# Kernel tuning notes

Measured on AMD Instinct MI355X. Metric: run time of the kernel, lower is better.

The kernel has to match this reference:

```python
import jax, jax.numpy as jnp
import numpy as np
import math

DIM = 1024
CHUNK = 64
B, S = 4, 4096

def setup_inputs() -> dict:
    key = jax.random.key(0)
    ks = jax.random.split(key, 16)
    d = DIM
    std = 1.0 / math.sqrt(d)
    def lin(k):
        k1, k2 = jax.random.split(k)
        return (jax.random.uniform(k1, (d, d), jnp.float32, -std, std),
                jax.random.uniform(k2, (d,), jnp.float32, -std, std))
    Wk, bk = lin(ks[0])
    Wv, bv = lin(ks[1])
    Wq, bq = lin(ks[2])
    Wkp, bkp = lin(ks[3])
    Wqp, bqp = lin(ks[4])
    Wo, bo = lin(ks[5])
    return {
        "x": jax.random.normal(ks[6], (B, S, d), jnp.float32),
        "Wk": Wk, "bk": bk, "Wv": Wv, "bv": bv, "Wq": Wq, "bq": bq,
        "Wkp": Wkp, "bkp": bkp, "Wqp": Wqp, "bqp": bqp,
        "phase_scale": jnp.full((d,), math.pi, jnp.float32),
        "ln_g": jnp.ones((d,), jnp.float32),
        "ln_b": jnp.zeros((d,), jnp.float32),
        "Wo": Wo, "bo": bo,
    }

def _linear(x, W, b):
    # torch nn.Linear: x @ W.T + b
    return jnp.einsum('bsd,ed->bse', x, W) + b

def _layernorm(x, g, b, eps=1e-5):
    mu = jnp.mean(x, axis=-1, keepdims=True)
    var = jnp.var(x, axis=-1, keepdims=True)
    return (x - mu) * jax.lax.rsqrt(var + eps) * g + b

def reference(x, Wk, bk, Wv, bv, Wq, bq, Wkp, bkp, Wqp, bqp,
              phase_scale, ln_g, ln_b, Wo, bo):
    batch, seq_len, dim = x.shape
    key = _linear(x, Wk, bk)
    value = _linear(x, Wv, bv)
    query = _linear(x, Wq, bq)
    key_phase = jnp.tanh(_linear(key, Wkp, bkp)) * phase_scale
    query_phase = jnp.tanh(_linear(query, Wqp, bqp)) * phase_scale
    bound_real = value * jnp.cos(key_phase)
    bound_imag = value * jnpp_sin(key_phase) if False else value * jnp.sin(key_phase)
    pad_len = (CHUNK - seq_len % CHUNK) % CHUNK
    if pad_len > 0:
        pad = ((0, 0), (0, pad_len), (0, 0))
        bound_real = jnp.pad(bound_real, pad)
        bound_imag = jnp.pad(bound_imag, pad)
        query_phase = jnp.pad(query_phase, pad)
    padded_len = bound_real.shape[1]
    nc = padded_len // CHUNK
    br = bound_real.reshape(batch, nc, CHUNK, dim)
    bi = bound_imag.reshape(batch, nc, CHUNK, dim)
    qp = query_phase.reshape(batch, nc, CHUNK, dim)
    mem_real = jnp.cumsum(br, axis=2)
    mem_imag = jnp.cumsum(bi, axis=2)
    retrieved = mem_real * jnp.cos(qp) + mem_imag * jnp.sin(qp)
    retrieved = retrieved.reshape(batch, padded_len, dim)[:, :seq_len]
    retrieved = retrieved / math.sqrt(dim)
    out = _linear(_layernorm(retrieved, ln_g, ln_b), Wo, bo)
    return x + out
```

## Files before the change

kernel.cpp:

```cpp
#include <hip/hip_runtime.h>
#include <math.h>

#define DIMD 1024
#define CHUNKLEN 64
#define NTOK 16384

#define TM 128
#define TN 128
#define BK 64

typedef __bf16 bf16x8 __attribute__((ext_vector_type(8)));
typedef float floatx4 __attribute__((ext_vector_type(4)));
typedef unsigned short ushort8v __attribute__((ext_vector_type(8)));

__device__ __forceinline__ float bf2f(unsigned short u) {
  union { unsigned int i; float f; } v; v.i = ((unsigned int)u) << 16; return v.f;
}
__device__ __forceinline__ unsigned short f2bf(float f) {
  union { float f; unsigned int i; } v; v.f = f;
  unsigned int r = v.i + 0x7FFFu + ((v.i >> 16) & 1u);
  return (unsigned short)(r >> 16);
}

__device__ __forceinline__ float tanh_fast(float v) {
  const float t = __expf(2.0f * v);
  return 1.0f - 2.0f * __builtin_amdgcn_rcpf(t + 1.0f);
}

__device__ __forceinline__ void async16(const unsigned short* g, unsigned short* l) {
  __builtin_amdgcn_global_load_lds(
      (const __attribute__((address_space(1))) unsigned int*)g,
      (__attribute__((address_space(3))) unsigned int*)l, 16, 0, 0);
}

__global__ __launch_bounds__(256) void cvt_all_kernel(
    const float* __restrict__ x,
    const float* __restrict__ w0, const float* __restrict__ w1,
    const float* __restrict__ w2, const float* __restrict__ w3,
    unsigned short* __restrict__ dx,
    unsigned short* __restrict__ d0, unsigned short* __restrict__ d1,
    unsigned short* __restrict__ d2, unsigned short* __restrict__ d3)
{
  const int b = blockIdx.x;
  const float* src; unsigned short* dst; long i;
  if (b < 16384) {
    src = x; dst = dx; i = (long)b * 256 + threadIdx.x;
  } else {
    const int r = b - 16384;
    const int s = r >> 10;
    src = s == 0 ? w0 : s == 1 ? w1 : s == 2 ? w2 : w3;
    dst = s == 0 ? d0 : s == 1 ? d1 : s == 2 ? d2 : d3;
    i = (long)(r & 1023) * 256 + threadIdx.x;
  }
  const float4 v = ((const float4*)src)[i];
  ushort4 o;
  o.x = f2bf(v.x); o.y = f2bf(v.y); o.z = f2bf(v.z); o.w = f2bf(v.w);
  ((ushort4*)dst)[i] = o;
}

__global__ __launch_bounds__(256) void transpose_cvt_kernel(
    const float* __restrict__ s0, const float* __restrict__ s1,
    unsigned short* __restrict__ q0, unsigned short* __restrict__ q1)
{
  __shared__ unsigned short tile[64][66];
  const float* src = blockIdx.z ? s1 : s0;
  unsigned short* dst = blockIdx.z ? q1 : q0;
  const int e0 = blockIdx.y * 64;
  const int k0 = blockIdx.x * 64;
  const int t  = threadIdx.x;
  const int tr = t >> 4;
  const int tc = t & 15;
#pragma unroll
  for (int p = 0; p < 4; ++p) {
    const int el = p * 16 + tr;
    const float4 v = *(const float4*)&src[(long)(e0 + el) * DIMD + k0 + tc * 4];
    tile[el][tc * 4 + 0] = f2bf(v.x);
    tile[el][tc * 4 + 1] = f2bf(v.y);
    tile[el][tc * 4 + 2] = f2bf(v.z);
    tile[el][tc * 4 + 3] = f2bf(v.w);
  }
  __syncthreads();
#pragma unroll
  for (int p = 0; p < 4; ++p) {
    const int kl = p * 16 + tr;
    ushort4 o;
    o.x = tile[tc * 4 + 0][kl];
    o.y = tile[tc * 4 + 1][kl];
    o.z = tile[tc * 4 + 2][kl];
    o.w = tile[tc * 4 + 3][kl];
    *(ushort4*)&dst[(long)(k0 + kl) * DIMD + e0 + tc * 4] = o;
  }
}

__global__ __launch_bounds__(256) void bias_comb_kernel(
    const float* __restrict__ Wkp, const float* __restrict__ bk,
    const float* __restrict__ bkp,
    const float* __restrict__ Wqp, const float* __restrict__ bq,
    const float* __restrict__ bqp,
    float* __restrict__ bkq, float* __restrict__ bqq)
{
  const int b = blockIdx.x;
  const int which = b >> 8;
  const int lane = threadIdx.x & 63;
  const int wid  = threadIdx.x >> 6;
  const int n = (b & 255) * 4 + wid;
  const float* W    = which ? Wqp : Wkp;
  const float* bvec = which ? bq  : bk;
  const float* badd = which ? bqp : bkp;
  float*       outp = which ? bqq : bkq;
  float s = 0.f;
#pragma unroll
  for (int i = 0; i < 16; ++i)
    s += W[(long)n * DIMD + lane + i * 64] * bvec[lane + i * 64];
#pragma unroll
  for (int o = 32; o > 0; o >>= 1) s += __shfl_xor(s, o, 64);
  if (lane == 0) outp[n] = s + badd[n];
}

template <int MODE>
__global__ __launch_bounds__(256) void gemm_bt_kernel(
    const unsigned short* __restrict__ A0, const unsigned short* __restrict__ A1,
    const unsigned short* __restrict__ W0, const unsigned short* __restrict__ W1,
    const unsigned short* __restrict__ W2,
    const float* __restrict__ b0, const float* __restrict__ b1,
    const float* __restrict__ b2,
    const float* __restrict__ aux,
    unsigned short* __restrict__ O0, unsigned short* __restrict__ O1,
    unsigned short* __restrict__ O2,
    float* __restrict__ Of, const float* __restrict__ resid)
{
  __shared__ unsigned short lsA[TM * BK];
  __shared__ unsigned short lsB[TN * BK];

  const int tid  = threadIdx.x;
  const int lane = tid & 63;
  const int wid  = tid >> 6;
  const long bm  = (long)blockIdx.y * TM;
  const long bng = (long)blockIdx.x * TN;

  const unsigned short* A = A0;
  const unsigned short* W = W0;
  const float* bias = b0;
  unsigned short* Ob = O0;
  long bn = bng;
  int seg = 0;
  if (MODE == 0) {
    seg = (int)(bng >> 10);
    bn = bng & 1023;
    W    = seg == 0 ? W0 : (seg == 1 ? W1 : W2);
    bias = seg == 0 ? b0 : (seg == 1 ? b1 : b2);
    Ob   = seg == 0 ? O0 : (seg == 1 ? O1 : O2);
  } else if (MODE == 1) {
    if (blockIdx.z) { A = A1; W = W1; Ob = O1; }
  }

  const int wm = (wid & 1) * 64;
  const int wn = (wid >> 1) * 64;

  floatx4 acc[4][4];
#pragma unroll
  for (int i = 0; i < 4; ++i)
#pragma unroll
    for (int j = 0; j < 4; ++j)
      acc[i][j] = (floatx4)(0.0f);

  const int srow  = lane >> 3;
  const int pcol  = (lane & 7) * 8;
  const int lcolL = (((lane & 7) ^ (srow & 7)) * 8);
  const int frm   = lane & 15;
  const int cfrk  = lane >> 4;

  for (int kk = 0; kk < DIMD; kk += BK) {
    __syncthreads();
#pragma unroll
    for (int j = 0; j < 4; ++j) {
      const int inst = wid * 4 + j;
      const int r = inst * 8 + srow;
      async16(A + (bm + r) * (long)DIMD + kk + lcolL, &lsA[r * BK + pcol]);
      async16(W + (bn + r) * (long)DIMD + kk + lcolL, &lsB[r * BK + pcol]);
    }
    __syncthreads();
#pragma unroll
    for (int ks = 0; ks < BK; ks += 32) {
      const int cb  = (ks >> 3) + cfrk;
      const int swz = ((cb ^ (frm & 7)) << 3);
      bf16x8 af[4], bfr[4];
#pragma unroll
      for (int i = 0; i < 4; ++i)
        af[i]  = *(const bf16x8*)&lsA[(wm + i * 16 + frm) * BK + swz];
#pragma unroll
      for (int i = 0; i < 4; ++i)
        bfr[i] = *(const bf16x8*)&lsB[(wn + i * 16 + frm) * BK + swz];
#pragma unroll
      for (int i = 0; i < 4; ++i)
#pragma unroll
        for (int j = 0; j < 4; ++j)
          acc[i][j] = __builtin_amdgcn_mfma_f32_16x16x32_bf16(af[i], bfr[j], acc[i][j], 0, 0, 0);
    }
  }

  const int cn = lane & 15;
  const int rq = (lane >> 4) * 4;
#pragma unroll
  for (int j = 0; j < 4; ++j) {
    const long col = bn + wn + j * 16 + cn;
    const float bv = (MODE == 1) ? 0.0f : bias[col];
    const float pv = (MODE == 0) ? aux[col] : 0.0f;
#pragma unroll
    for (int i = 0; i < 4; ++i) {
#pragma unroll
      for (int r = 0; r < 4; ++r) {
        const long row = bm + wm + i * 16 + rq + r;
        const float v = acc[i][j][r] + bv;
        if (MODE == 0) {
          Ob[row * (long)DIMD + col] = (seg == 0) ? f2bf(v)
                                                  : f2bf(tanh_fast(v) * pv);
        } else if (MODE == 1) {
          Ob[row * (long)DIMD + col] = f2bf(v);
        } else {
          Of[row * (long)DIMD + col] = v + resid[row * (long)DIMD + col];
        }
      }
    }
  }
}

#define TILE16 16384
#define HALF16 8192

template <int MODE>
__global__ __launch_bounds__(512, 2) void gemm256_kernel(
    const unsigned short* __restrict__ A,
    const unsigned short* __restrict__ W0, const unsigned short* __restrict__ W1,
    const unsigned short* __restrict__ W2,
    const float* __restrict__ b0, const float* __restrict__ b1,
    const float* __restrict__ b2,
    const float* __restrict__ aux,
    unsigned short* __restrict__ O0, unsigned short* __restrict__ O1,
    unsigned short* __restrict__ O2,
    float* __restrict__ Of, const float* __restrict__ resid)
{
  __shared__ unsigned short lds[4 * TILE16];

  const int tid  = threadIdx.x;
  const int lane = tid & 63;
  const int wid  = tid >> 6;

  constexpr int NBX = (MODE == 0) ? 12 : 4;
  constexpr int NWG = NBX * 64;
  const int orig = blockIdx.x + blockIdx.y * gridDim.x;
  const int swzb = (orig & 7) * (NWG >> 3) + (orig >> 3);
  const int nb = swzb % NBX;
  const int mb = swzb / NBX;

  const long bm = (long)mb * 256;
  long bn;
  int seg = 0;
  const unsigned short* W = W0;
  const float* bias = b0;
  unsigned short* Ob = O0;
  if (MODE == 0) {
    seg = nb >> 2;
    bn  = (long)(nb & 3) * 256;
    W    = seg == 0 ? W0 : (seg == 1 ? W1 : W2);
    bias = seg == 0 ? b0 : (seg == 1 ? b1 : b2);
    Ob   = seg == 0 ? O0 : (seg == 1 ? O1 : O2);
  } else {
    bn = (long)nb * 256;
  }

  const int wm = (wid >> 2) * 128;
  const int wn = (wid & 3) * 64;

  const int q0  = wid * 2;
  const int sr0 = q0 * 16 + (lane >> 2);
  const int sg  = (((lane & 3) ^ ((sr0 >> 1) & 3)) * 8);
  const int sd0 = q0 * 512 + lane * 8;
  const long arow = (bm + sr0) * (long)DIMD;
  const long brow = (bn + sr0) * (long)DIMD;

  const int frm   = lane & 15;
  const int cfrk  = lane >> 4;
  const int slot8 = (cfrk ^ ((frm >> 1) & 3)) * 8;
  const int rbase = frm * 32 + slot8;

  floatx4 acc[8][4];
#pragma unroll
  for (int i = 0; i < 8; ++i)
#pragma unroll
    for (int j = 0; j < 4; ++j) acc[i][j] = (floatx4)(0.0f);

  bf16x8 bfr[4];

#define SA256(buf, kk, h) do { \
    const unsigned short* _s = A + arow + (kk) + (h) * 32 + sg; \
    unsigned short* _d = &lds[(buf) * TILE16 + (h) * HALF16 + sd0]; \
    async16(_s, _d); \
    async16(_s + 16 * DIMD, _d + 512); \
  } while (0)
#define SB256(buf, kk, h) do { \
    const unsigned short* _s = W + brow + (kk) + (h) * 32 + sg; \
    unsigned short* _d = &lds[2 * TILE16 + (buf) * TILE16 + (h) * HALF16 + sd0]; \
    async16(_s, _d); \
    async16(_s + 16 * DIMD, _d + 512); \
  } while (0)
#define RDA256(buf, h, ih, af) do { \
    const int _ab = (buf) * TILE16 + (h) * HALF16 + (wm + (ih) * 64) * 32 + rbase; \
    _Pragma("unroll") \
    for (int _i = 0; _i < 4; ++_i) (af)[_i] = *(const bf16x8*)&lds[_ab + _i * 512]; \
  } while (0)
#define RDB256(buf, h) do { \
    const int _bb = 2 * TILE16 + (buf) * TILE16 + (h) * HALF16 + wn * 32 + rbase; \
    _Pragma("unroll") \
    for (int _j = 0; _j < 4; ++_j) bfr[_j] = *(const bf16x8*)&lds[_bb + _j * 512]; \
  } while (0)
#define VMW4() asm volatile("s_waitcnt vmcnt(4)" ::: "memory")
#define BAR256() do { \
    asm volatile("" ::: "memory"); \
    __builtin_amdgcn_s_barrier(); \
    asm volatile("" ::: "memory"); \
  } while (0)
#define LG0() do { \
    asm volatile("s_waitcnt lgkmcnt(0)" ::: "memory"); \
    __builtin_amdgcn_sched_barrier(0); \
  } while (0)
#define MFMA16(ih, af) do { \
    __builtin_amdgcn_s_setprio(1); \
    _Pragma("unroll") \
    for (int _i = 0; _i < 4; ++_i) \
      _Pragma("unroll") \
      for (int _j = 0; _j < 4; ++_j) \
        acc[(ih) * 4 + _i][_j] = __builtin_amdgcn_mfma_f32_16x16x32_bf16( \
            (af)[_i], bfr[_j], acc[(ih) * 4 + _i][_j], 0, 0, 0); \
    __builtin_amdgcn_s_setprio(0); \
  } while (0)

  SA256(0, 0, 0); SB256(0, 0, 0); SA256(0, 0, 1); SB256(0, 0, 1);
  VMW4();
  BAR256();

#pragma unroll 1
  for (int t = 0; t < 16; t += 2) {
    const int k1 = (t + 1) * 64;
    const int k2 = (t + 2 < 16) ? (t + 2) * 64 : 0;
    {
      { bf16x8 af[4]; RDA256(0, 0, 0, af); RDB256(0, 0); SA256(1, k1, 0);
        BAR256(); LG0(); MFMA16(0, af); BAR256(); }
      { bf16x8 af[4]; RDA256(0, 0, 1, af); SB256(1, k1, 0); VMW4();
        BAR256(); LG0(); MFMA16(1, af); BAR256(); }
      { bf16x8 af[4]; RDA256(0, 1, 0, af); RDB256(0, 1); SA256(1, k1, 1);
        BAR256(); LG0(); MFMA16(0, af); BAR256(); }
      { bf16x8 af[4]; RDA256(0, 1, 1, af); SB256(1, k1, 1); VMW4();
        BAR256(); LG0(); MFMA16(1, af); BAR256(); }
      { bf16x8 af[4]; RDA256(1, 0, 0, af); RDB256(1, 0); SA256(0, k2, 0);
        BAR256(); LG0(); MFMA16(0, af); BAR256(); }
      { bf16x8 af[4]; RDA256(1, 0, 1, af); SB256(0, k2, 0); VMW4();
        BAR256(); LG0(); MFMA16(1, af); BAR256(); }
      { bf16x8 af[4]; RDA256(1, 1, 0, af); RDB256(1, 1); SA256(0, k2, 1);
        BAR256(); LG0(); MFMA16(0, af); BAR256(); }
      { bf16x8 af[4]; RDA256(1, 1, 1, af); SB256(0, k2, 1); VMW4();
        BAR256(); LG0(); MFMA16(1, af); BAR256(); }
    }
  }
  asm volatile("s_waitcnt vmcnt(0)" ::: "memory");

#undef SA256
#undef SB256
#undef RDA256
#undef RDB256
#undef VMW4
#undef BAR256
#undef LG0
#undef MFMA16

  const int cn = lane & 15;
  const int rq = (lane >> 4) * 4;
  long colj[4]; float bvj[4], pvj[4];
#pragma unroll
  for (int j = 0; j < 4; ++j) {
    colj[j] = bn + wn + j * 16 + cn;
    bvj[j]  = bias[colj[j]];
    pvj[j]  = (MODE == 0) ? aux[colj[j]] : 0.0f;
  }
#pragma unroll
  for (int ii = 0; ii < 8; ++ii) {
#pragma unroll
    for (int r = 0; r < 4; ++r) {
      const long rowo = (bm + wm + ii * 16 + rq + r) * (long)DIMD;
#pragma unroll
      for (int j = 0; j < 4; ++j) {
        const float v = acc[ii][j][r] + bvj[j];
        if (MODE == 0) {
          Ob[rowo + colj[j]] = (seg == 0) ? f2bf(v)
                                          : f2bf(tanh_fast(v) * pvj[j]);
        } else {
          Of[rowo + colj[j]] = v + resid[rowo + colj[j]];
        }
      }
    }
  }
}

__global__ __launch_bounds__(512) void scan_ln_kernel(
    const unsigned short* __restrict__ V,  const unsigned short* __restrict__ KP,
    const unsigned short* __restrict__ QP,
    const float* __restrict__ lng, const float* __restrict__ lnb,
    unsigned short* __restrict__ out)
{
  __shared__ unsigned short ret_s[32][DIMD];

  const int tid  = threadIdx.x;
  const int lane = tid & 63;
  const int wid  = tid >> 6;
  const long rowBase = (long)blockIdx.x * CHUNKLEN;
  const int d0 = tid * 2;

  const int c0 = lane * 8;
  const int c1 = 512 + lane * 8;
  float g0[8], be0[8], g1[8], be1[8];
#pragma unroll
  for (int j = 0; j < 8; ++j) {
    g0[j] = lng[c0 + j]; be0[j] = lnb[c0 + j];
    g1[j] = lng[c1 + j]; be1[j] = lnb[c1 + j];
  }

  float mr[2] = {0.f, 0.f};
  float mi[2] = {0.f, 0.f};

  for (int h = 0; h < 2; ++h) {
    for (int tl = 0; tl < 32; ++tl) {
      const int t = h * 32 + tl;
      const long off = (rowBase + t) * DIMD + d0;
      const ushort2 v2 = *(const ushort2*)(V + off);
      const ushort2 k2 = *(const ushort2*)(KP + off);
      const ushort2 q2 = *(const ushort2*)(QP + off);
      const unsigned short va[2] = {v2.x, v2.y};
      const unsigned short ka[2] = {k2.x, k2.y};
      const unsigned short qa[2] = {q2.x, q2.y};
      unsigned short rv[2];
#pragma unroll
      for (int j = 0; j < 2; ++j) {
        const float v  = bf2f(va[j]);
        const float kp = bf2f(ka[j]);
        const float qp = bf2f(qa[j]);
        float skp, ckp, sqp, cqp;
        __sincosf(kp, &skp, &ckp);
        __sincosf(qp, &sqp, &cqp);
        mr[j] += v * ckp;
        mi[j] += v * skp;
        rv[j] = f2bf((mr[j] * cqp + mi[j] * sqp) * 0.03125f);
      }
      ushort2 o2; o2.x = rv[0]; o2.y = rv[1];
      *(ushort2*)&ret_s[tl][d0] = o2;
    }
    __syncthreads();

#pragma unroll 1
    for (int rr = 0; rr < 4; ++rr) {
      const int tl = wid * 4 + rr;
      const ushort8v a0 = *(const ushort8v*)&ret_s[tl][c0];
      const ushort8v a1 = *(const ushort8v*)&ret_s[tl][c1];
      float f0[8], f1[8];
      float s = 0.f, s2 = 0.f;
#pragma unroll
      for (int j = 0; j < 8; ++j) {
        f0[j] = bf2f(a0[j]); f1[j] = bf2f(a1[j]);
        s += f0[j] + f1[j];
        s2 += f0[j] * f0[j] + f1[j] * f1[j];
      }
#pragma unroll
      for (int o = 32; o > 0; o >>= 1) {
        s  += __shfl_xor(s,  o, 64);
        s2 += __shfl_xor(s2, o, 64);
      }
      const float mu  = s * (1.0f / DIMD);
      const float var = s2 * (1.0f / DIMD) - mu * mu;
      const float inv = rsqrtf(var + 1e-5f);
      ushort8v o0, o1;
#pragma unroll
      for (int j = 0; j < 8; ++j) {
        o0[j] = f2bf((f0[j] - mu) * inv * g0[j] + be0[j]);
        o1[j] = f2bf((f1[j] - mu) * inv * g1[j] + be1[j]);
      }
      const long gro = (rowBase + h * 32 + tl) * DIMD;
      *(ushort8v*)(out + gro + c0) = o0;
      *(ushort8v*)(out + gro + c1) = o1;
    }
    __syncthreads();
  }
}

extern "C" void kernel_launch(void* const* d_in, const int* in_sizes, int n_in,
                              void* d_out, int out_size, void* d_ws, size_t ws_size,
                              hipStream_t stream)
{
  const float* x   = (const float*)d_in[0];
  const float* Wk  = (const float*)d_in[1];
  const float* bk  = (const float*)d_in[2];
  const float* Wv  = (const float*)d_in[3];
  const float* bv  = (const float*)d_in[4];
  const float* Wq  = (const float*)d_in[5];
  const float* bq  = (const float*)d_in[6];
  const float* Wkp = (const float*)d_in[7];
  const float* bkp = (const float*)d_in[8];
  const float* Wqp = (const float*)d_in[9];
  const float* bqp = (const float*)d_in[10];
  const float* ph  = (const float*)d_in[11];
  const float* lng = (const float*)d_in[12];
  const float* lnb = (const float*)d_in[13];
  const float* Wo  = (const float*)d_in[14];
  const float* bo  = (const float*)d_in[15];
  float* out = (float*)d_out;

  const long NB = (long)NTOK * DIMD;
  const long DD = (long)DIMD * DIMD;
  const size_t required = (size_t)(4 * NB + 8 * DD) * sizeof(unsigned short)
                        + 2048 * sizeof(float);
  if (ws_size < required) return;

  unsigned short* S0   = (unsigned short*)d_ws;
  unsigned short* SV   = S0   + NB;
  unsigned short* SKP  = SV   + NB;
  unsigned short* SQP  = SKP  + NB;
  unsigned short* Wvb  = SQP  + NB;
  unsigned short* Wob  = Wvb  + DD;
  unsigned short* Wkpb = Wob  + DD;
  unsigned short* Wqpb = Wkpb + DD;
  unsigned short* WkT  = Wqpb + DD;
  unsigned short* WqT  = WkT  + DD;
  unsigned short* Wkqb = WqT  + DD;
  unsigned short* Wqqb = Wkqb + DD;
  float* bkq = (float*)(Wqqb + DD);
  float* bqq = bkq + DIMD;

  dim3 blk(256);

  cvt_all_kernel<<<dim3(16384 + 4 * 1024), blk, 0, stream>>>(
      x, Wv, Wo, Wkp, Wqp, S0, Wvb, Wob, Wkpb, Wqpb);
  transpose_cvt_kernel<<<dim3(16, 16, 2), blk, 0, stream>>>(Wk, Wq, WkT, WqT);
  bias_comb_kernel<<<dim3(512), blk, 0, stream>>>(Wkp, bk, bkp, Wqp, bq, bqp, bkq, bqq);
  gemm_bt_kernel<1><<<dim3(DIMD / TN, DIMD / TM, 2), blk, 0, stream>>>(
      Wkpb, Wqpb, WkT, WqT, nullptr, nullptr, nullptr, nullptr, nullptr,
      Wkqb, Wqqb, nullptr, nullptr, nullptr);
  gemm256_kernel<0><<<dim3(12, NTOK / 256), dim3(512), 0, stream>>>(
      S0, Wvb, Wkqb, Wqqb, bv, bkq, bqq, ph, SV, SKP, SQP, nullptr, nullptr);
  scan_ln_kernel<<<dim3(NTOK / CHUNKLEN), dim3(512), 0, stream>>>(
      SV, SKP, SQP, lng, lnb, S0);
  gemm256_kernel<2><<<dim3(4, NTOK / 256), dim3(512), 0, stream>>>(
      S0, Wob, nullptr, nullptr, bo, nullptr, nullptr, nullptr,
      nullptr, nullptr, nullptr, out, x);
}
```

Baseline: 360.6 us.

## Cut per-substep barriers in 256-thread GEMM main loop to two per K half

The GEMM main loop used to issue two workgroup barriers plus an lgkmcnt(0) wait and a sched_barrier around every MFMA sub-block, which is 16 barriers per K tile. The new KTILE macro removes the explicit LDS waits and keeps a single barrier after each pair of sub-blocks, once the global-to-LDS loads have landed. This lets the compiler interleave LDS reads with MFMAs and reduces stall time at synchronisation points. The cost is weaker ordering guarantees: fewer barriers between reading a buffer and overwriting it could cause LDS read/write hazards if the async stores land in a buffer other waves are still reading.

```diff
diff --git a/kernel.cpp b/kernel.cpp
--- a/kernel.cpp
+++ b/kernel.cpp
@@ -320,10 +320,6 @@
     __builtin_amdgcn_s_barrier(); \
     asm volatile("" ::: "memory"); \
   } while (0)
-#define LG0() do { \
-    asm volatile("s_waitcnt lgkmcnt(0)" ::: "memory"); \
-    __builtin_amdgcn_sched_barrier(0); \
-  } while (0)
 #define MFMA16(ih, af) do { \
     __builtin_amdgcn_s_setprio(1); \
     _Pragma("unroll") \
@@ -334,6 +330,16 @@
             (af)[_i], bfr[_j], acc[(ih) * 4 + _i][_j], 0, 0, 0); \
     __builtin_amdgcn_s_setprio(0); \
   } while (0)
+#define KTILE(c, n, kn) do { \
+    { bf16x8 af[4]; RDA256(c, 0, 0, af); RDB256(c, 0); \
+      SA256(n, kn, 0); MFMA16(0, af); } \
+    { bf16x8 af[4]; RDA256(c, 0, 1, af); \
+      SB256(n, kn, 0); VMW4(); BAR256(); MFMA16(1, af); } \
+    { bf16x8 af[4]; RDA256(c, 1, 0, af); RDB256(c, 1); \
+      SA256(n, kn, 1); MFMA16(0, af); } \
+    { bf16x8 af[4]; RDA256(c, 1, 1, af); \
+      SB256(n, kn, 1); VMW4(); BAR256(); MFMA16(1, af); } \
+  } while (0)
 
   SA256(0, 0, 0); SB256(0, 0, 0); SA256(0, 0, 1); SB256(0, 0, 1);
   VMW4();
@@ -343,24 +349,8 @@
   for (int t = 0; t < 16; t += 2) {
     const int k1 = (t + 1) * 64;
     const int k2 = (t + 2 < 16) ? (t + 2) * 64 : 0;
-    {
-      { bf16x8 af[4]; RDA256(0, 0, 0, af); RDB256(0, 0); SA256(1, k1, 0);
-        BAR256(); LG0(); MFMA16(0, af); BAR256(); }
-      { bf16x8 af[4]; RDA256(0, 0, 1, af); SB256(1, k1, 0); VMW4();
-        BAR256(); LG0(); MFMA16(1, af); BAR256(); }
-      { bf16x8 af[4]; RDA256(0, 1, 0, af); RDB256(0, 1); SA256(1, k1, 1);
-        BAR256(); LG0(); MFMA16(0, af); BAR256(); }
-      { bf16x8 af[4]; RDA256(0, 1, 1, af); SB256(1, k1, 1); VMW4();
-        BAR256(); LG0(); MFMA16(1, af); BAR256(); }
-      { bf16x8 af[4]; RDA256(1, 0, 0, af); RDB256(1, 0); SA256(0, k2, 0);
-        BAR256(); LG0(); MFMA16(0, af); BAR256(); }
-      { bf16x8 af[4]; RDA256(1, 0, 1, af); SB256(0, k2, 0); VMW4();
-        BAR256(); LG0(); MFMA16(1, af); BAR256(); }
-      { bf16x8 af[4]; RDA256(1, 1, 0, af); RDB256(1, 1); SA256(0, k2, 1);
-        BAR256(); LG0(); MFMA16(0, af); BAR256(); }
-      { bf16x8 af[4]; RDA256(1, 1, 1, af); SB256(0, k2, 1); VMW4();
-        BAR256(); LG0(); MFMA16(1, af); BAR256(); }
-    }
+    KTILE(0, 1, k1);
+    KTILE(1, 0, k2);
   }
   asm volatile("s_waitcnt vmcnt(0)" ::: "memory");
 
@@ -370,8 +360,8 @@
 #undef RDB256
 #undef VMW4
 #undef BAR256
-#undef LG0
 #undef MFMA16
+#undef KTILE
 
   const int cn = lane & 15;
   const int rq = (lane >> 4) * 4;
```

Result: no change. 358.9 us (-0.5%).
